# Kernel optimization log

Hardware: AMD Instinct MI355X
Metric: run time of the kernel (lower is better)

## Reference

```python
import jax, jax.numpy as jnp
import numpy as np

H, W = 16, 16  # input_resolution
NUM_HEADS = 16
DIM = 512


def build_relative_position_index(h, w):
    coords = np.stack(np.meshgrid(np.arange(h), np.arange(w), indexing='ij'))  # [2,h,w]
    cf = coords.reshape(2, -1)
    rel = cf[:, :, None] - cf[:, None, :]            # [2,N,N]
    rel = rel.transpose(1, 2, 0).astype(np.int32)    # [N,N,2]
    rel[:, :, 0] += h - 1
    rel[:, :, 1] += w - 1
    rel[:, :, 0] *= 2 * w - 1
    return jnp.asarray(rel.sum(-1).reshape(-1), dtype=jnp.int32)  # [N*N]


def setup_inputs() -> dict:
    key = jax.random.key(0)
    ks = jax.random.split(key, 6)
    B, N, C = 128, H * W, DIM
    x = jax.random.normal(ks[0], (B, N, C), dtype=jnp.float32)
    qkv_w = jax.random.normal(ks[1], (3 * C, C), dtype=jnp.float32) * (C ** -0.5)
    qkv_b = jax.random.normal(ks[2], (3 * C,), dtype=jnp.float32) * 0.02
    proj_w = jax.random.normal(ks[3], (C, C), dtype=jnp.float32) * (C ** -0.5)
    proj_b = jax.random.normal(ks[4], (C,), dtype=jnp.float32) * 0.02
    bias_table = jax.random.normal(ks[5], ((2 * H - 1) * (2 * W - 1), NUM_HEADS), dtype=jnp.float32) * 0.02
    rel_index = build_relative_position_index(H, W)
    return {"x": x, "qkv_w": qkv_w, "qkv_b": qkv_b, "proj_w": proj_w,
            "proj_b": proj_b, "bias_table": bias_table, "rel_index": rel_index}


def reference(x, qkv_w, qkv_b, proj_w, proj_b, bias_table, rel_index):
    B, N, C = x.shape
    h = NUM_HEADS
    hd = C // h
    scale = hd ** -0.5
    # qkv projection: [B,N,3C] -> [3,B,h,N,hd]
    qkv = (jnp.einsum('bnc,oc->bno', x, qkv_w) + qkv_b)
    qkv = qkv.reshape(B, N, 3, h, hd).transpose(2, 0, 3, 1, 4)
    q, k, v = qkv[0], qkv[1], qkv[2]
    # relative position bias: gather [N*N,h] -> [1,h,N,N]
    bias = bias_table[rel_index].reshape(N, N, h).transpose(2, 0, 1)[None]
    attn = jnp.einsum('bhnd,bhmd->bhnm', q * scale, k) + bias
    attn = jax.nn.softmax(attn, axis=-1)
    out = jnp.einsum('bhnm,bhmd->bhnd', attn, v)     # [B,h,N,hd]
    out = out.transpose(0, 2, 1, 3).reshape(B, N, C)
    return jnp.einsum('bnc,oc->bno', out, proj_w) + proj_b
```

## Files before the change

### kernel.cpp

```cpp
#include <hip/hip_runtime.h>

typedef __bf16 bf16_t;
typedef __bf16 bf16x8 __attribute__((ext_vector_type(8)));
typedef float f32x4 __attribute__((ext_vector_type(4)));

#define MFMA_16x16x32(a, b, c) __builtin_amdgcn_mfma_f32_16x16x32_bf16((a), (b), (c), 0, 0, 0)

__device__ inline bf16x8 cvt8(const float* __restrict__ p) {
  bf16x8 r;
#pragma unroll
  for (int j = 0; j < 8; j++) r[j] = (bf16_t)p[j];
  return r;
}

__device__ inline void load_lds16(const bf16_t* g, bf16_t* l) {
  __builtin_amdgcn_global_load_lds(
      (const __attribute__((address_space(1))) void*)g,
      (__attribute__((address_space(3))) void*)l, 16, 0, 0);
}

__global__ __launch_bounds__(256) void convert_k(
    const float* __restrict__ x, const float* __restrict__ qkv_w,
    const float* __restrict__ proj_w,
    bf16_t* __restrict__ xbf, bf16_t* __restrict__ wqkvbf,
    bf16_t* __restrict__ wprojbf) {
  size_t base = ((size_t)blockIdx.x * 256 + threadIdx.x) * 8;
  if (base < 16777216) {
    *(bf16x8*)(xbf + base) = cvt8(x + base);
  } else if (base < 17563648) {
    size_t o = base - 16777216;
    *(bf16x8*)(wqkvbf + o) = cvt8(qkv_w + o);
  } else {
    size_t o = base - 17563648;
    *(bf16x8*)(wprojbf + o) = cvt8(proj_w + o);
  }
}

__global__ __launch_bounds__(256) void bias_gather_k(
    const float* __restrict__ table, const int* __restrict__ rel,
    float* __restrict__ biasws) {
  int idx = blockIdx.x * 256 + threadIdx.x;
  int h = idx >> 16;
  int rem = idx & 65535;
  int rb = rem >> 12;
  int ct = (rem >> 8) & 15;
  int L = (rem >> 2) & 63;
  int r = idx & 3;
  int row = rb * 16 + (L >> 4) * 4 + r;
  int col = ct * 16 + (L & 15);
  biasws[idx] = table[rel[row * 256 + col] * 16 + h];
}

__global__ __launch_bounds__(256) void qkv_gemm128_k(
    const bf16_t* __restrict__ A, const bf16_t* __restrict__ W,
    const float* __restrict__ Bvec,
    bf16_t* __restrict__ qws, bf16_t* __restrict__ kws, bf16_t* __restrict__ vws) {
  __shared__ bf16_t As[128 * 32];
  __shared__ bf16_t Bs[128 * 32];
  const int id = blockIdx.x;
  const int xcd = id & 7;
  const int j = id >> 3;
  const int mt = (j / 12) * 8 + xcd;
  const int nt = j % 12;
  const int m0 = mt * 128;
  const int n0 = nt * 128;
  const int t = threadIdx.x;
  const int w = t >> 6, L = t & 63;
  const int lrow = L & 15, lq = L >> 4;
  const int rw = (w & 1) * 64, cw = (w >> 1) * 64;
  const int srow = w * 32 + (L >> 2);
  const int skoff = (L & 3) * 8;

  f32x4 acc[4][4] = {};
  for (int k0 = 0; k0 < 512; k0 += 32) {
    load_lds16(A + (size_t)(m0 + srow) * 512 + k0 + skoff, As + w * 1024);
    load_lds16(A + (size_t)(m0 + 16 + srow) * 512 + k0 + skoff, As + w * 1024 + 512);
    load_lds16(W + (size_t)(n0 + srow) * 512 + k0 + skoff, Bs + w * 1024);
    load_lds16(W + (size_t)(n0 + 16 + srow) * 512 + k0 + skoff, Bs + w * 1024 + 512);
    __syncthreads();
    bf16x8 af[4], bf[4];
#pragma unroll
    for (int i = 0; i < 4; i++) {
      af[i] = *(const bf16x8*)&As[(rw + i * 16 + lrow) * 32 + lq * 8];
      bf[i] = *(const bf16x8*)&Bs[(cw + i * 16 + lrow) * 32 + lq * 8];
    }
#pragma unroll
    for (int i = 0; i < 4; i++)
#pragma unroll
      for (int jj = 0; jj < 4; jj++)
        acc[i][jj] = MFMA_16x16x32(af[i], bf[jj], acc[i][jj]);
    __syncthreads();
  }

  const float scale = 0.17677669529663687f;
#pragma unroll
  for (int jj = 0; jj < 4; jj++) {
    int o = n0 + cw + jj * 16 + lrow;
    int s = o >> 9, rem = o & 511, hh = rem >> 5, d = rem & 31;
    float bias = Bvec[o];
    bf16_t* dst = (s == 0) ? qws : (s == 1) ? kws : vws;
    float mul = (s == 0) ? scale : 1.0f;
#pragma unroll
    for (int i = 0; i < 4; i++)
#pragma unroll
      for (int r = 0; r < 4; r++) {
        int m = m0 + rw + i * 16 + lq * 4 + r;
        int b = m >> 8, n = m & 255;
        float val = (acc[i][jj][r] + bias) * mul;
        dst[(size_t)(((b * 16 + hh) * 256 + n) << 5) + d] = (bf16_t)val;
      }
  }
}

__global__ __launch_bounds__(256) void proj_gemm128_k(
    const bf16_t* __restrict__ A, const bf16_t* __restrict__ W,
    const float* __restrict__ Bvec, float* __restrict__ out) {
  __shared__ bf16_t As[128 * 32];
  __shared__ bf16_t Bs[128 * 32];
  const int id = blockIdx.x;
  const int xcd = id & 7;
  const int j = id >> 3;
  const int mt = (j >> 2) * 8 + xcd;
  const int nt = j & 3;
  const int m0 = mt * 128;
  const int n0 = nt * 128;
  const int t = threadIdx.x;
  const int w = t >> 6, L = t & 63;
  const int lrow = L & 15, lq = L >> 4;
  const int rw = (w & 1) * 64, cw = (w >> 1) * 64;
  const int srow = w * 32 + (L >> 2);
  const int skoff = (L & 3) * 8;

  f32x4 acc[4][4] = {};
  for (int k0 = 0; k0 < 512; k0 += 32) {
    load_lds16(A + (size_t)(m0 + srow) * 512 + k0 + skoff, As + w * 1024);
    load_lds16(A + (size_t)(m0 + 16 + srow) * 512 + k0 + skoff, As + w * 1024 + 512);
    load_lds16(W + (size_t)(n0 + srow) * 512 + k0 + skoff, Bs + w * 1024);
    load_lds16(W + (size_t)(n0 + 16 + srow) * 512 + k0 + skoff, Bs + w * 1024 + 512);
    __syncthreads();
    bf16x8 af[4], bf[4];
#pragma unroll
    for (int i = 0; i < 4; i++) {
      af[i] = *(const bf16x8*)&As[(rw + i * 16 + lrow) * 32 + lq * 8];
      bf[i] = *(const bf16x8*)&Bs[(cw + i * 16 + lrow) * 32 + lq * 8];
    }
#pragma unroll
    for (int i = 0; i < 4; i++)
#pragma unroll
      for (int jj = 0; jj < 4; jj++)
        acc[i][jj] = MFMA_16x16x32(af[i], bf[jj], acc[i][jj]);
    __syncthreads();
  }

#pragma unroll
  for (int jj = 0; jj < 4; jj++) {
    int o = n0 + cw + jj * 16 + lrow;
    float bias = Bvec[o];
#pragma unroll
    for (int i = 0; i < 4; i++)
#pragma unroll
      for (int r = 0; r < 4; r++) {
        int m = m0 + rw + i * 16 + lq * 4 + r;
        out[(size_t)m * 512 + o] = acc[i][jj][r] + bias;
      }
  }
}

__global__ __launch_bounds__(256) void attn_k(
    const bf16_t* __restrict__ qws, const bf16_t* __restrict__ kws,
    const bf16_t* __restrict__ vws, const float* __restrict__ biasws,
    bf16_t* __restrict__ aows) {
  __shared__ __align__(16) char smem[33792 + 16896];
  bf16_t* Ps = (bf16_t*)smem;
  bf16_t* Vs = (bf16_t*)(smem + 33792);

  const int id = blockIdx.x;
  const int xcd = id & 7;
  const int jj = id >> 3;
  const int bh = (jj >> 2) * 8 + xcd;
  const int strip = jj & 3;
  const int h = bh & 15, b = bh >> 4;

  const int t = threadIdx.x;
  const int w = t >> 6, L = t & 63;
  const int lrow = L & 15, lq = L >> 4;

  const bf16_t* kbase = kws + (size_t)bh * 8192;
  const bf16_t* vbase = vws + (size_t)bh * 8192;
#pragma unroll
  for (int c = 0; c < 4; c++) {
    bf16x8 vv = *(const bf16x8*)(vbase + t * 32 + c * 8);
#pragma unroll
    for (int j = 0; j < 8; j++) Vs[(c * 8 + j) * 264 + t] = vv[j];
  }

  const bf16_t* qbase = qws + (size_t)bh * 8192 + (strip * 64 + w * 16) * 32;
  bf16x8 qf = *(const bf16x8*)(qbase + lrow * 32 + lq * 8);
  bf16x8 kf[16];
#pragma unroll
  for (int ct = 0; ct < 16; ct++)
    kf[ct] = *(const bf16x8*)(kbase + (ct * 16 + lrow) * 32 + lq * 8);

  const float* bb = biasws + h * 65536 + (strip * 4 + w) * 4096;
  f32x4 S[16];
#pragma unroll
  for (int ct = 0; ct < 16; ct++) {
    f32x4 bi = *(const f32x4*)(bb + ct * 256 + L * 4);
    S[ct] = MFMA_16x16x32(qf, kf[ct], bi);
  }

  float sm[4] = {0.f, 0.f, 0.f, 0.f};
#pragma unroll
  for (int ct = 0; ct < 16; ct++)
#pragma unroll
    for (int r = 0; r < 4; r++) {
      float e = __expf(S[ct][r]);
      S[ct][r] = e;
      sm[r] += e;
    }
#pragma unroll
  for (int r = 0; r < 4; r++)
#pragma unroll
    for (int msk = 1; msk < 16; msk <<= 1)
      sm[r] += __shfl_xor(sm[r], msk, 64);
  float inv[4];
#pragma unroll
  for (int r = 0; r < 4; r++) inv[r] = 1.0f / sm[r];

  bf16_t* Pw = Ps + w * 4224;
#pragma unroll
  for (int ct = 0; ct < 16; ct++)
#pragma unroll
    for (int r = 0; r < 4; r++)
      Pw[(lq * 4 + r) * 264 + ct * 16 + lrow] = (bf16_t)S[ct][r];

  __syncthreads();

  f32x4 O0 = {}, O1 = {};
#pragma unroll
  for (int c = 0; c < 8; c++) {
    bf16x8 pf = *(const bf16x8*)&Pw[lrow * 264 + c * 32 + lq * 8];
    bf16x8 v0 = *(const bf16x8*)&Vs[lrow * 264 + c * 32 + lq * 8];
    bf16x8 v1 = *(const bf16x8*)&Vs[(16 + lrow) * 264 + c * 32 + lq * 8];
    O0 = MFMA_16x16x32(pf, v0, O0);
    O1 = MFMA_16x16x32(pf, v1, O1);
  }
  bf16_t* obase = aows + (size_t)(b * 256 + strip * 64 + w * 16) * 512 + h * 32;
#pragma unroll
  for (int r = 0; r < 4; r++) {
    int rl = lq * 4 + r;
    obase[rl * 512 + lrow] = (bf16_t)(O0[r] * inv[r]);
    obase[rl * 512 + 16 + lrow] = (bf16_t)(O1[r] * inv[r]);
  }
}

extern "C" void kernel_launch(void* const* d_in, const int* in_sizes, int n_in,
                              void* d_out, int out_size, void* d_ws, size_t ws_size,
                              hipStream_t stream) {
  (void)in_sizes; (void)n_in; (void)out_size; (void)ws_size;
  const float* x      = (const float*)d_in[0];
  const float* qkv_w  = (const float*)d_in[1];
  const float* qkv_b  = (const float*)d_in[2];
  const float* proj_w = (const float*)d_in[3];
  const float* proj_b = (const float*)d_in[4];
  const float* table  = (const float*)d_in[5];
  const int*   rel    = (const int*)d_in[6];

  const size_t QKV_ELEMS = 16777216;
  bf16_t* qws     = (bf16_t*)d_ws;
  bf16_t* kws     = qws + QKV_ELEMS;
  bf16_t* vws     = kws + QKV_ELEMS;
  float*  biasws  = (float*)(vws + QKV_ELEMS);
  bf16_t* wqkvbf  = (bf16_t*)(biasws + 1048576);
  bf16_t* wprojbf = wqkvbf + 786432;
  bf16_t* xbf     = wprojbf + 262144;
  bf16_t* aows    = xbf;
  float*  out     = (float*)d_out;

  convert_k<<<8704, 256, 0, stream>>>(x, qkv_w, proj_w, xbf, wqkvbf, wprojbf);
  bias_gather_k<<<4096, 256, 0, stream>>>(table, rel, biasws);
  qkv_gemm128_k<<<3072, 256, 0, stream>>>(xbf, wqkvbf, qkv_b, qws, kws, vws);
  attn_k<<<8192, 256, 0, stream>>>(qws, kws, vws, biasws, aows);
  proj_gemm128_k<<<1024, 256, 0, stream>>>(aows, wprojbf, proj_b, out);
}
```

Measured before the change: 289.2 us.

## Replace 128x128 projection GEMMs with pipelined 256x256 double-buffered LDS kernel

Both the QKV and output-projection GEMMs move to a shared 256x256-tile core with 512 threads. The core uses double-buffered, XOR-swizzled LDS fed by direct global-to-LDS loads. It interleaves prefetch of the next K slices with MFMA phases, using explicit barriers, waitcnt and s_setprio to overlap memory with compute. Larger tiles raise data reuse and cut the number of workgroups, but the 128KB of LDS limits occupancy to one block per CU.

```diff
diff --git a/kernel.cpp b/kernel.cpp
--- a/kernel.cpp
+++ b/kernel.cpp
@@ -51,118 +51,198 @@
   biasws[idx] = table[rel[row * 256 + col] * 16 + h];
 }
 
-__global__ __launch_bounds__(256) void qkv_gemm128_k(
+#define PH_MID()                                          \
+  do {                                                    \
+    __builtin_amdgcn_s_barrier();                         \
+    asm volatile("s_waitcnt lgkmcnt(0)" ::: "memory");    \
+    __builtin_amdgcn_sched_barrier(0);                    \
+    __builtin_amdgcn_s_setprio(1);                        \
+  } while (0)
+
+#define PH_END()                                          \
+  do {                                                    \
+    __buil_noop();                                        \
+  } while (0)
+
+__device__ __forceinline__ void __builtin_dummy() {}
+#undef PH_END
+#define PH_END()                                          \
+  do {                                                    \
+    __builtin_amdgcn_s_setprio(0);                        \
+    __builtin_amdgcn_s_barrier();                         \
+    __builtin_amdgcn_sched_barrier(0);                    \
+  } while (0)
+
+#define STGA(buf, tl, c)                                                         \
+  do {                                                                           \
+    load_lds16(ga + (size_t)(tl)*64 + (c)*32768, la + (buf)*16384 + (c)*4096);   \
+    load_lds16(ga + (size_t)(tl)*64 + ((c) + 1) * 32768,                         \
+               la + (buf)*16384 + ((c) + 1) * 4096);                             \
+  } while (0)
+#define STGB(buf, tl, c)                                                         \
+  do {                                                                           \
+    load_lds16(gb + (size_t)(tl)*64 + (c)*32768, lb + (buf)*16384 + (c)*4096);   \
+    load_lds16(gb + (size_t)(tl)*64 + ((c) + 1) * 32768,                         \
+               lb + (buf)*16384 + ((c) + 1) * 4096);                             \
+  } while (0)
+
+#define RDA(dst, buf, ibase)                                                     \
+  _Pragma("unroll") for (int i = 0; i < 4; ++i) {                                \
+    dst[i][0] = *(const bf16x8*)&As[(buf)*16384 + a0 + ((ibase) + i) * 1024];    \
+    dst[i][1] = *(const bf16x8*)&As[(buf)*16384 + a1 + ((ibase) + i) * 1024];    \
+  }
+#define RDB(dst, buf, jbase)                                                     \
+  _Pragma("unroll") for (int j = 0; j < 2; ++j) {                                \
+    dst[j][0] = *(const bf16x8*)&Bs[(buf)*16384 + b0 + ((jbase) + j) * 1024];    \
+    dst[j][1] = *(const bf16x8*)&Bs[(buf)*16384 + b1 + ((jbase) + j) * 1024];    \
+  }
+
+#define MFQ(Af, Bf, I0, J0)                                                      \
+  _Pragma("unroll") for (int i = 0; i < 4; ++i) _Pragma("unroll")                \
+      for (int j = 0; j < 2; ++j) {                                              \
+    acc[(I0) + i][(J0) + j] =                                                    \
+        MFMA_16x16x32(Af[i][0], Bf[j][0], acc[(I0) + i][(J0) + j]);              \
+    acc[(I0) + i][(J0) + j] =                                                    \
+        MFMA_16x16x32(Af[i][1], Bf[j][1], acc[(I0) + i][(J0) + j]);              \
+  }
+
+__device__ __forceinline__ void gemm256_core(
+    const bf16_t* __restrict__ Ap, const bf16_t* __restrict__ Wp,
+    int m0, int n0, f32x4 (&acc)[8][4]) {
+  __shared__ bf16_t As[2 * 16384];
+  __shared__ bf16_t Bs[2 * 16384];
+  const int t = threadIdx.x;
+  const int w = t >> 6, L = t & 63;
+  const int wm = w >> 2, wn = w & 3;
+  const int lrow = L & 15, lq = L >> 4;
+
+  const int srow = t >> 3;
+  const int sslot = (t & 7) ^ (srow & 7);
+  const bf16_t* ga = Ap + (size_t)(m0 + srow) * 512 + sslot * 8;
+  const bf16_t* gb = Wp + (size_t)(n0 + srow) * 512 + sslot * 8;
+  bf16_t* la = As + t * 8;
+  bf16_t* lb = Bs + t * 8;
+
+  const int m8 = (lrow & 7) * 8;
+  const int a0 = (wm * 128 + lrow) * 64 + ((lq * 8) ^ m8);
+  const int a1 = (wm * 128 + lrow) * 64 + ((32 + lq * 8) ^ m8);
+  const int b0 = (wn * 64 + lrow) * 64 + ((lq * 8) ^ m8);
+  const int b1 = (wn * 64 + lrow) * 64 + ((32 + lq * 8) ^ m8);
+
+  STGA(0, 0, 0); STGA(0, 0, 2); STGB(0, 0, 0); STGB(0, 0, 2);
+  STGA(1, 1, 0); STGA(1, 1, 2); STGB(1, 1, 0); STGB(1, 1, 2);
+  asm volatile("s_waitcnt vmcnt(8)" ::: "memory");
+  __builtin_amdgcn_s_barrier();
+  __builtin_amdgcn_sched_barrier(0);
+
+#pragma unroll
+  for (int it = 0; it < 4; ++it) {
+    {
+      bf16x8 fal[4][2], fah[4][2], fbl[2][2], fbh[2][2];
+      RDA(fal, 0, 0); RDB(fbl, 0, 0);
+      if (it > 0) STGB(1, 2 * it + 1, 0);
+      PH_MID(); MFQ(fal, fbl, 0, 0); PH_END();
+      RDA(fah, 0, 4); RDB(fbh, 0, 2);
+      if (it > 0) STGB(1, 2 * it + 1, 2);
+      PH_MID(); MFQ(fah, fbh, 4, 2); PH_END();
+      if (it < 3) STGA(0, 2 * it + 2, 0);
+      PH_MID(); MFQ(fal, fbh, 0, 2); PH_END();
+      if (it < 3) STGA(0, 2 * it + 2, 2);
+      PH_MID(); MFQ(fah, fbl, 4, 0);
+      __builtin_amdgcn_s_setprio(0);
+      if (it < 3) asm volatile("s_waitcnt vmcnt(4)" ::: "memory");
+      else        asm volatile("s_waitcnt vmcnt(0)" ::: "memory");
+      __builtin_amdgcn_s_barrier();
+      __builtin_amdgcn_sched_barrier(0);
+    }
+    {
+      bf16x8 fal[4][2], fah[4][2], fbl[2][2], fbh[2][2];
+      RDA(fal, 1, 0); RDB(fbl, 1, 0);
+      if (it < 3) STGB(0, 2 * it + 2, 0);
+      PH_MID(); MFQ(fal, fbl, 0, 0); PH_END();
+      RDA(fah, 1, 4); RDB(fbh, 1, 2);
+      if (it < 3) STGB(0, 2 * it + 2, 2);
+      PH_MID(); MFQ(fah, fbh, 4, 2); PH_END();
+      if (it < 3) STGA(1, 2 * it + 3, 0);
+      PH_MID(); MFQ(fal, fbh, 0, 2); PH_END();
+      if (it < 3) STGA(1, 2 * it + 3, 2);
+      PH_MID(); MFQ(fah, fbl, 4, 0);
+      __builtin_amdgcn_s_setprio(0);
+      if (it < 3) {
+        asm volatile("s_waitcnt vmcnt(4)" ::: "memory");
+        __builtin_amdgcn_s_barrier();
+        __builtin_amdgcn_sched_barrier(0);
+      }
+    }
+  }
+}
+
+__global__ __launch_bounds__(512, 2) void qkv_gemm256_k(
     const bf16_t* __restrict__ A, const bf16_t* __restrict__ W,
     const float* __restrict__ Bvec,
     bf16_t* __restrict__ qws, bf16_t* __restrict__ kws, bf16_t* __restrict__ vws) {
-  __shared__ bf16_t As[128 * 32];
-  __shared__ bf16_t Bs[128 * 32];
   const int id = blockIdx.x;
-  const int xcd = id & 7;
-  const int j = id >> 3;
-  const int mt = (j / 12) * 8 + xcd;
-  const int nt = j % 12;
-  const int m0 = mt * 128;
-  const int n0 = nt * 128;
+  const int wg = (id & 7) * 96 + (id >> 3);
+  const int mt = wg / 6, nt = wg % 6;
+  const int m0 = mt * 256, n0 = nt * 256;
+
+  f32x4 acc[8][4] = {};
+  gemm256_core(A, W, m0, n0, acc);
+
   const int t = threadIdx.x;
   const int w = t >> 6, L = t & 63;
+  const int wm = w >> 2, wn = w & 3;
   const int lrow = L & 15, lq = L >> 4;
-  const int rw = (w & 1) * 64, cw = (w >> 1) * 64;
-  const int srow = w * 32 + (L >> 2);
-  const int skoff = (L & 3) * 8;
-
-  f32x4 acc[4][4] = {};
-  for (int k0 = 0; k0 < 512; k0 += 32) {
-    load_lds16(A + (size_t)(m0 + srow) * 512 + k0 + skoff, As + w * 1024);
-    load_lds16(A + (size_t)(m0 + 16 + srow) * 512 + k0 + skoff, As + w * 1024 + 512);
-    load_lds16(W + (size_t)(n0 + srow) * 512 + k0 + skoff, Bs + w * 1024);
-    load_lds16(W + (size_t)(n0 + 16 + srow) * 512 + k0 + skoff, Bs + w * 1024 + 512);
-    __syncthreads();
-    bf16x8 af[4], bf[4];
-#pragma unroll
-    for (int i = 0; i < 4; i++) {
-      af[i] = *(const bf16x8*)&As[(rw + i * 16 + lrow) * 32 + lq * 8];
-      bf[i] = *(const bf16x8*)&Bs[(cw + i * 16 + lrow) * 32 + lq * 8];
-    }
-#pragma unroll
-    for (int i = 0; i < 4; i++)
-#pragma unroll
-      for (int jj = 0; jj < 4; jj++)
-        acc[i][jj] = MFMA_16x16x32(af[i], bf[jj], acc[i][jj]);
-    __syncthreads();
-  }
-
-  const float scale = 0.17677669529663687f;
-#pragma unroll
-  for (int jj = 0; jj < 4; jj++) {
-    int o = n0 + cw + jj * 16 + lrow;
-    int s = o >> 9, rem = o & 511, hh = rem >> 5, d = rem & 31;
+  const int col0 = n0 + wn * 64;
+  const int s = col0 >> 9;
+  bf16_t* dst = (s == 0) ? qws : (s == 1) ? kws : vws;
+  const float mul = (s == 0) ? 0.17677669529663687f : 1.0f;
+#pragma unroll
+  for (int jj = 0; jj < 4; ++jj) {
+    int o = col0 + jj * 16 + lrow;
     float bias = Bvec[o];
-    bf16_t* dst = (s == 0) ? qws : (s == 1) ? kws : vws;
-    float mul = (s == 0) ? scale : 1.0f;
-#pragma unroll
-    for (int i = 0; i < 4; i++)
-#pragma unroll
-      for (int r = 0; r < 4; r++) {
-        int m = m0 + rw + i * 16 + lq * 4 + r;
+    int rem = o & 511;
+    int hh = rem >> 5, d = rem & 31;
+#pragma unroll
+    for (int i = 0; i < 8; ++i) {
+#pragma unroll
+      for (int r = 0; r < 4; ++r) {
+        int m = m0 + wm * 128 + i * 16 + lq * 4 + r;
         int b = m >> 8, n = m & 255;
-        float val = (acc[i][jj][r] + bias) * mul;
-        dst[(size_t)(((b * 16 + hh) * 256 + n) << 5) + d] = (bf16_t)val;
+        dst[(size_t)(((b * 16 + hh) * 256 + n) << 5) + d] =
+            (bf16_t)((acc[i][jj][r] + bias) * mul);
       }
-  }
-}
-
-__global__ __launch_bounds__(256) void proj_gemm128_k(
+    }
+  }
+}
+
+__global__ __launch_bounds__(512, 2) void proj_gemm256_k(
     const bf16_t* __restrict__ A, const bf16_t* __restrict__ W,
     const float* __restrict__ Bvec, float* __restrict__ out) {
-  __shared__ bf16_t As[128 * 32];
-  __shared__ bf16_t Bs[128 * 32];
   const int id = blockIdx.x;
-  const int xcd = id & 7;
-  const int j = id >> 3;
-  const int mt = (j >> 2) * 8 + xcd;
-  const int nt = j & 3;
-  const int m0 = mt * 128;
-  const int n0 = nt * 128;
+  const int wg = (id & 7) * 32 + (id >> 3);
+  const int mt = wg >> 1, nt = wg & 1;
+  const int m0 = mt * 256, n0 = nt * 256;
+
+  f32x4 acc[8][4] = {};
+  gemm256_core(A, W, m0, n0, acc);
+
   const int t = threadIdx.x;
   const int w = t >> 6, L = t & 63;
+  const int wm = w >> 2, wn = w & 3;
   const int lrow = L & 15, lq = L >> 4;
-  const int rw = (w & 1) * 64, cw = (w >> 1) * 64;
-  const int srow = w * 32 + (L >> 2);
-  const int skoff = (L & 3) * 8;
-
-  f32x4 acc[4][4] = {};
-  for (int k0 = 0; k0 < 512; k0 += 32) {
-    load_lds16(A + (size_t)(m0 + srow) * 512 + k0 + skoff, As + w * 1024);
-    load_lds16(A + (size_t)(m0 + 16 + srow) * 512 + k0 + skoff, As + w * 1024 + 512);
-    load_lds16(W + (size_t)(n0 + srow) * 512 + k0 + skoff, Bs + w * 1024);
-    load_lds16(W + (size_t)(n0 + 16 + srow) * 512 + k0 + skoff, Bs + w * 1024 + 512);
-    __syncthreads();
-    bf16x8 af[4], bf[4];
-#pragma unroll
-    for (int i = 0; i < 4; i++) {
-      af[i] = *(const bf16x8*)&As[(rw + i * 16 + lrow) * 32 + lq * 8];
-      bf[i] = *(const bf16x8*)&Bs[(cw + i * 16 + lrow) * 32 + lq * 8];
-    }
-#pragma unroll
-    for (int i = 0; i < 4; i++)
-#pragma unroll
-      for (int jj = 0; jj < 4; jj++)
-        acc[i][jj] = MFMA_16x16x32(af[i], bf[jj], acc[i][jj]);
-    __syncthreads();
-  }
-
-#pragma unroll
-  for (int jj = 0; jj < 4; jj++) {
-    int o = n0 + cw + jj * 16 + lrow;
+#pragma unroll
+  for (int jj = 0; jj < 4; ++jj) {
+    int o = n0 + wn * 64 + jj * 16 + lrow;
     float bias = Bvec[o];
 #pragma unroll
-    for (int i = 0; i < 4; i++)
-#pragma unroll
-      for (int r = 0; r < 4; r++) {
-        int m = m0 + rw + i * 16 + lq * 4 + r;
+    for (int i = 0; i < 8; ++i) {
+#pragma unroll
+      for (int r = 0; r < 4; ++r) {
+        int m = m0 + wm * 128 + i * 16 + lq * 4 + r;
         out[(size_t)m * 512 + o] = acc[i][jj][r] + bias;
       }
+    }
   }
 }
 
@@ -279,7 +359,7 @@
 
   convert_k<<<8704, 256, 0, stream>>>(x, qkv_w, proj_w, xbf, wqkvbf, wprojbf);
   bias_gather_k<<<4096, 256, 0, stream>>>(table, rel, biasws);
-  qkv_gemm128_k<<<3072, 256, 0, stream>>>(xbf, wqkvbf, qkv_b, qws, kws, vws);
+  qkv_gemm256_k<<<768, 512, 0, stream>>>(xbf, wqkvbf, qkv_b, qws, kws, vws);
   attn_k<<<8192, 256, 0, stream>>>(qws, kws, vws, biasws, aows);
-  proj_gemm128_k<<<1024, 256, 0, stream>>>(aows, wprojbf, proj_b, out);
-}
+  proj_gemm256_k<<<256, 512, 0, stream>>>(aows, wprojbf, proj_b, out);
+}
```

Measured after the change: 292.7 us. No clear change (+1.2%).
